# Optimization experiments

Measured on AMD Instinct MI355X. Metric: run time of the kernel, lower is better.

## Reference

```python
import jax, jax.numpy as jnp
import numpy as np
import math

INPUT_DIM = 256
HIDDEN_DIM = 128
N = 8192
GATE_TEMPERATURE = 1.0
LN_EPS = 1e-5


def setup_inputs() -> dict:
    key = jax.random.key(0)
    ks = jax.random.split(key, 10)
    s_in = 1.0 / math.sqrt(INPUT_DIM)
    s_h = 1.0 / math.sqrt(HIDDEN_DIM)
    s_cat = 1.0 / math.sqrt(INPUT_DIM + HIDDEN_DIM)
    return {
        "node_features": jax.random.normal(ks[0], (N, INPUT_DIM), jnp.float32),
        "adj_matrix": jax.random.uniform(ks[1], (N, N), jnp.float32),
        "msg_w": jax.random.uniform(ks[2], (INPUT_DIM, HIDDEN_DIM), jnp.float32, -s_in, s_in),
        "msg_b": jax.random.uniform(ks[3], (HIDDEN_DIM,), jnp.float32, -s_in, s_in),
        "upd_w": jax.random.uniform(ks[4], (INPUT_DIM + HIDDEN_DIM, HIDDEN_DIM), jnp.float32, -s_cat, s_cat),
        "upd_b": jax.random.uniform(ks[5], (HIDDEN_DIM,), jnp.float32, -s_cat, s_cat),
        "gate_q_w": jax.random.uniform(ks[6], (HIDDEN_DIM, HIDDEN_DIM), jnp.float32, -s_h, s_h),
        "gate_k_w": jax.random.uniform(ks[7], (HIDDEN_DIM, HIDDEN_DIM), jnp.float32, -s_h, s_h),
        "gate_bias": jnp.float32(-1.0),
        "ln_gamma": jnp.ones((HIDDEN_DIM,), jnp.float32),
        "ln_beta": jnp.zeros((HIDDEN_DIM,), jnp.float32),
    }


def reference(node_features, adj_matrix, msg_w, msg_b, upd_w, upd_b,
              gate_q_w, gate_k_w, gate_bias, ln_gamma, ln_beta):
    # messages: [N, hidden]
    messages = node_features @ msg_w + msg_b
    # edge gates: sigmoid(QK^T / (sqrt(d)*tau) + b), masked by adjacency
    q = messages @ gate_q_w  # [N, hidden]
    k = messages @ gate_k_w  # [N, hidden]
    scale = 1.0 / (math.sqrt(HIDDEN_DIM) * max(GATE_TEMPERATURE, 1e-6))
    scores = (q @ k.T) * scale  # [N, N]
    gates_masked = jax.nn.sigmoid(scores + gate_bias) * adj_matrix
    aggregated = gates_masked @ messages  # [N, hidden]
    combined = jnp.concatenate([node_features, aggregated], axis=1)
    updated = jax.nn.relu(combined @ upd_w + upd_b)
    # LayerNorm over last dim
    mu = jnp.mean(updated, axis=-1, keepdims=True)
    var = jnp.var(updated, axis=-1, keepdims=True)
    normed = (updated - mu) * jax.lax.rsqrt(var + LN_EPS)
    return normed * ln_gamma + ln_beta
```

## Files before the change

### kernel.cpp

```cpp
#include <hip/hip_runtime.h>
#include <hip/hip_bf16.h>
#include <stdint.h>

#define NN 8192
#define DIN 256
#define HID 128
#define SCALE 0.08838834764831845f

typedef __attribute__((ext_vector_type(8))) short short8;
typedef __attribute__((ext_vector_type(4))) float f32x4;
typedef __attribute__((ext_vector_type(8))) unsigned short u16x8;
typedef __attribute__((ext_vector_type(4))) unsigned short u16x4;

__device__ __forceinline__ unsigned short f2bf(float f) {
  unsigned int u = __builtin_bit_cast(unsigned int, f);
  u += 0x7FFFu + ((u >> 16) & 1u);
  return (unsigned short)(u >> 16);
}

__device__ __forceinline__ void async16(const void* g, void* l) {
  __builtin_amdgcn_global_load_lds(
      (const __attribute__((address_space(1))) unsigned int*)g,
      (__attribute__((address_space(3))) unsigned int*)l, 16, 0, 0);
}

__global__ __launch_bounds__(256) void kw0(
    const float* __restrict__ msg_w, const float* __restrict__ qw,
    const float* __restrict__ kw, const float* __restrict__ upd_w,
    unsigned short* __restrict__ mwT, unsigned short* __restrict__ qwT,
    unsigned short* __restrict__ kwT, unsigned short* __restrict__ w_t) {
  int idx0 = blockIdx.x * 1792 + threadIdx.x;
#pragma unroll
  for (int it = 0; it < 7; ++it) {
    int idx = idx0 + it * 256;
    if (idx < 32768) {
      int h = idx >> 8, j = idx & 255;
      mwT[idx] = f2bf(msg_w[j * HID + h]);
    } else if (idx < 49152) {
      int r = idx - 32768, h = r >> 7, j = r & 127;
      qwT[r] = f2bf(qw[j * HID + h]);
    } else if (idx < 65536) {
      int r = idx - 49152, h = r >> 7, j = r & 127;
      kwT[r] = f2bf(kw[j * HID + h]);
    } else {
      int r = idx - 65536, h = r / 384, j = r % 384;
      w_t[r] = f2bf(upd_w[j * HID + h]);
    }
  }
}

__global__ __launch_bounds__(256) void ka(
    const float* __restrict__ nf, const unsigned short* __restrict__ mwT,
    const float* __restrict__ msg_b, const unsigned short* __restrict__ qwT,
    const unsigned short* __restrict__ kwT, unsigned short* __restrict__ q_bf,
    unsigned short* __restrict__ k_bf, unsigned short* __restrict__ m_t,
    unsigned short* __restrict__ nf_bf) {
  __shared__ __align__(16) unsigned short nfl[32][264];
  __shared__ __align__(16) unsigned short ml[32][136];
  int t = threadIdx.x, l = t & 63, w = t >> 6;
  int lr = l & 15, lg = l >> 4;
  int i0 = blockIdx.x * 32;
  {
    int row = t >> 3, c0 = (t & 7) * 32;
    const float* src = nf + (size_t)(i0 + row) * DIN + c0;
    unsigned short* gdst = nf_bf + (size_t)(i0 + row) * DIN + c0;
#pragma unroll
    for (int v = 0; v < 4; ++v) {
      f32x4 a = *(const f32x4*)(src + v * 8);
      f32x4 b = *(const f32x4*)(src + v * 8 + 4);
      u16x8 o;
#pragma unroll
      for (int e = 0; e < 4; ++e) { o[e] = f2bf(a[e]); o[4 + e] = f2bf(b[e]); }
      *(u16x8*)&nfl[row][c0 + v * 8] = o;
      *(u16x8*)(gdst + v * 8) = o;
    }
  }
  __syncthreads();
  int rl = (w >> 1) * 16;
  int nb = (w & 1) * 4;
  f32x4 macc[4];
#pragma unroll
  for (int nt = 0; nt < 4; ++nt) macc[nt] = (f32x4){0.f, 0.f, 0.f, 0.f};
#pragma unroll
  for (int kk = 0; kk < 8; ++kk) {
    short8 af = *(const short8*)&nfl[rl + lr][kk * 32 + lg * 8];
#pragma unroll
    for (int nt = 0; nt < 4; ++nt) {
      short8 bf = *(const short8*)(mwT + (size_t)((nb + nt) * 16 + lr) * DIN + kk * 32 + lg * 8);
      macc[nt] = __builtin_amdgcn_mfma_f32_16x16x32_bf16(af, bf, macc[nt], 0, 0, 0);
    }
  }
#pragma unroll
  for (int nt = 0; nt < 4; ++nt) {
    int col = (nb + nt) * 16 + lr;
    float bias = msg_b[col];
#pragma unroll
    for (int reg = 0; reg < 4; ++reg)
      ml[rl + lg * 4 + reg][col] = f2bf(macc[nt][reg] + bias);
  }
  __syncthreads();
  {
    int hh = t >> 1, i8 = (t & 1) * 16;
    u16x8 o0, o1;
#pragma unroll
    for (int v = 0; v < 8; ++v) { o0[v] = ml[i8 + v][hh]; o1[v] = ml[i8 + 8 + v][hh]; }
    *(u16x8*)(m_t + (size_t)hh * NN + i0 + i8) = o0;
    *(u16x8*)(m_t + (size_t)hh * NN + i0 + i8 + 8) = o1;
  }
  f32x4 qacc[4], kacc[4];
#pragma unroll
  for (int nt = 0; nt < 4; ++nt) {
    qacc[nt] = (f32x4){0.f, 0.f, 0.f, 0.f};
    kacc[nt] = (f32x4){0.f, 0.f, 0.f, 0.f};
  }
#pragma unroll
  for (int kk = 0; kk < 4; ++kk) {
    short8 af = *(const short8*)&ml[rl + lr][kk * 32 + lg * 8];
#pragma unroll
    for (int nt = 0; nt < 4; ++nt) {
      short8 bq = *(const short8*)(qwT + (size_t)((nb + nt) * 16 + lr) * HID + kk * 32 + lg * 8);
      short8 bk = *(const short8*)(kwT + (size_t)((nb + nt) * 16 + lr) * HID + kk * 32 + lg * 8);
      qacc[nt] = __builtin_amdgcn_mfma_f32_16x16x32_bf16(af, bq, qacc[nt], 0, 0, 0);
      kacc[nt] = __builtin_amdgcn_mfma_f32_16x16x32_bf16(af, bk, kacc[nt], 0, 0, 0);
    }
  }
#pragma unroll
  for (int nt = 0; nt < 4; ++nt) {
    int col = (nb + nt) * 16 + lr;
#pragma unroll
    for (int reg = 0; reg < 4; ++reg) {
      int row = i0 + rl + lg * 4 + reg;
      q_bf[(size_t)row * HID + col] = f2bf(qacc[nt][reg]);
      k_bf[(size_t)row * HID + col] = f2bf(kacc[nt][reg]);
    }
  }
}

__global__ __launch_bounds__(256, 4) void kb(
    const unsigned short* __restrict__ q_bf, const unsigned short* __restrict__ k_bf,
    const unsigned short* __restrict__ m_t, const float* __restrict__ adj,
    const float* __restrict__ gate_bias, float* __restrict__ agg_parts) {
  __shared__ __align__(16) char klds[16384];
  __shared__ __align__(16) char mlds[16384];
  __shared__ __align__(16) char glds[8192];
  int t = threadIdx.x, l = t & 63, w = t >> 6;
  int lr = l & 15, lg = l >> 4;
  int lin = blockIdx.x + blockIdx.y * 128;
  int nlin = (lin & 7) * 128 + (lin >> 3);
  int bx = nlin & 127, by = nlin >> 7;
  int i0 = bx * 64;
  int jbase = by * 1024;
  float gb = gate_bias[0];

  int qrow = i0 + w * 16 + lr;
  short8 qf[4];
#pragma unroll
  for (int kk = 0; kk < 4; ++kk)
    qf[kk] = *(const short8*)(q_bf + (size_t)qrow * HID + kk * 32 + lg * 8);

  f32x4 acc[8];
#pragma unroll
  for (int nt = 0; nt < 8; ++nt) acc[nt] = (f32x4){0.f, 0.f, 0.f, 0.f};

  for (int jt = 0; jt < 16; ++jt) {
    int j0 = jbase + jt * 64;
    __syncthreads();
    float adjv[4][4];
#pragma unroll
    for (int jt16 = 0; jt16 < 4; ++jt16)
#pragma unroll
      for (int reg = 0; reg < 4; ++reg)
        adjv[jt16][reg] =
            adj[(size_t)(i0 + w * 16 + lg * 4 + reg) * NN + j0 + jt16 * 16 + lr];
#pragma unroll
    for (int p = 0; p < 4; ++p) {
      int row = p * 16 + (t >> 4);
      int lb = (t & 15) ^ (row & 7);
      async16(k_bf + (size_t)(j0 + row) * HID + lb * 8, klds + p * 4096 + w * 1024);
    }
#pragma unroll
    for (int p = 0; p < 4; ++p) {
      int row = p * 32 + (t >> 3);
      int lb = (t & 7) ^ (row & 7);
      async16(m_t + (size_t)row * NN + j0 + lb * 8, mlds + p * 4096 + w * 1024);
    }
    __syncthreads();

#pragma unroll
    for (int jt16 = 0; jt16 < 4; ++jt16) {
      f32x4 s_acc = (f32x4){0.f, 0.f, 0.f, 0.f};
#pragma unroll
      for (int kk = 0; kk < 4; ++kk) {
        int row = jt16 * 16 + lr;
        int blk = kk * 4 + lg;
        const short8 bf = *(const short8*)(klds + row * 256 + ((blk ^ (row & 7)) * 16));
        s_acc = __builtin_amdgcn_mfma_f32_16x16x32_bf16(qf[kk], bf, s_acc, 0, 0, 0);
      }
#pragma unroll
      for (int reg = 0; reg < 4; ++reg) {
        float x = s_acc[reg] * SCALE + gb;
        float e = __expf(-x);
        float g = adjv[jt16][reg] * __builtin_amdgcn_rcpf(1.0f + e);
        int row = lg * 4 + reg;
        int colb = (jt16 * 16 + lr) * 2;
        *(unsigned short*)(glds + w * 2048 + row * 128 + (colb ^ ((row & 7) << 4))) =
            f2bf(g);
      }
    }
#pragma unroll
    for (int kk2 = 0; kk2 < 2; ++kk2) {
      short8 af = *(const short8*)(glds + w * 2048 + lr * 128 +
                                   ((kk2 * 64 + lg * 16) ^ ((lr & 7) << 4)));
#pragma unroll
      for (int nt = 0; nt < 8; ++nt) {
        int mrow = nt * 16 + lr;
        int blk = kk2 * 4 + lg;
        const short8 bf =
            *(const short8*)(mlds + mrow * 128 + ((blk ^ (mrow & 7)) * 16));
        acc[nt] = __builtin_amdgcn_mfma_f32_16x16x32_bf16(af, bf, acc[nt], 0, 0, 0);
      }
    }
  }
  float* part = agg_parts + (size_t)by * NN * HID;
#pragma unroll
  for (int nt = 0; nt < 8; ++nt)
#pragma unroll
    for (int reg = 0; reg < 4; ++reg)
      part[(size_t)(i0 + w * 16 + lg * 4 + reg) * HID + nt * 16 + lr] = acc[nt][reg];
}

__global__ __launch_bounds__(256) void kc(
    const unsigned short* __restrict__ nf_bf, const float* __restrict__ agg_parts,
    const unsigned short* __restrict__ w_t, const float* __restrict__ upd_b,
    const float* __restrict__ gamma, const float* __restrict__ beta,
    float* __restrict__ out) {
  __shared__ __align__(16) unsigned short aggl[64][136];
  int t = threadIdx.x, l = t & 63, w = t >> 6;
  int i0 = blockIdx.x * 64;
  {
    const f32x4* p0 = (const f32x4*)(agg_parts + (size_t)i0 * HID);
    const size_t ps = (size_t)NN * HID / 4;
    for (int e = t; e < 64 * HID / 4; e += 256) {
      f32x4 s = p0[e];
#pragma unroll
      for (int c = 1; c < 8; ++c) s += p0[e + c * ps];
      int row = (e * 4) / HID, col = (e * 4) % HID;
      u16x4 o;
#pragma unroll
      for (int v = 0; v < 4; ++v) o[v] = f2bf(s[v]);
      *(u16x4*)&aggl[row][col] = o;
    }
  }
  __syncthreads();
  int lr = l & 15, lg = l >> 4;
  int arow = i0 + w * 16 + lr;
  short8 af[12];
#pragma unroll
  for (int kk = 0; kk < 8; ++kk)
    af[kk] = *(const short8*)(nf_bf + (size_t)arow * DIN + kk * 32 + lg * 8);
#pragma unroll
  for (int kk = 8; kk < 12; ++kk)
    af[kk] = *(const short8*)(&aggl[w * 16 + lr][(kk - 8) * 32 + lg * 8]);
  f32x4 acc[8];
#pragma unroll
  for (int nt = 0; nt < 8; ++nt) acc[nt] = (f32x4){0.f, 0.f, 0.f, 0.f};
#pragma unroll
  for (int kk = 0; kk < 12; ++kk)
#pragma unroll
    for (int nt = 0; nt < 8; ++nt) {
      const short8 bf =
          *(const short8*)(w_t + (size_t)(nt * 16 + lr) * 384 + kk * 32 + lg * 8);
      acc[nt] = __builtin_amdgcn_mfma_f32_16x16x32_bf16(af[kk], bf, acc[nt], 0, 0, 0);
    }
  float ub[8], ga[8], be[8];
#pragma unroll
  for (int nt = 0; nt < 8; ++nt) {
    ub[nt] = upd_b[nt * 16 + lr];
    ga[nt] = gamma[nt * 16 + lr];
    be[nt] = beta[nt * 16 + lr];
  }
  float v[8][4], sum[4], sq[4];
#pragma unroll
  for (int reg = 0; reg < 4; ++reg) { sum[reg] = 0.f; sq[reg] = 0.f; }
#pragma unroll
  for (int nt = 0; nt < 8; ++nt)
#pragma unroll
    for (int reg = 0; reg < 4; ++reg) {
      float x = acc[nt][reg] + ub[nt];
      x = fmaxf(x, 0.f);
      v[nt][reg] = x;
      sum[reg] += x;
      sq[reg] = fmaf(x, x, sq[reg]);
    }
#pragma unroll
  for (int reg = 0; reg < 4; ++reg) {
#pragma unroll
    for (int m = 1; m < 16; m <<= 1) {
      sum[reg] += __shfl_xor(sum[reg], m, 16);
      sq[reg] += __shfl_xor(sq[reg], m, 16);
    }
  }
#pragma unroll
  for (int reg = 0; reg < 4; ++reg) {
    float mu = sum[reg] * (1.0f / 128.0f);
    float var = sq[reg] * (1.0f / 128.0f) - mu * mu;
    float rstd = rsqrtf(var + 1e-5f);
    int orow = i0 + w * 16 + lg * 4 + reg;
#pragma unroll
    for (int nt = 0; nt < 8; ++nt) {
      float y = (v[nt][reg] - mu) * rstd * ga[nt] + be[nt];
      out[(size_t)orow * HID + nt * 16 + lr] = y;
    }
  }
}

extern "C" void kernel_launch(void* const* d_in, const int* in_sizes, int n_in,
                              void* d_out, int out_size, void* d_ws, size_t ws_size,
                              hipStream_t stream) {
  const float* nf    = (const float*)d_in[0];
  const float* adj   = (const float*)d_in[1];
  const float* msg_w = (const float*)d_in[2];
  const float* msg_b = (const float*)d_in[3];
  const float* upd_w = (const float*)d_in[4];
  const float* upd_b = (const float*)d_in[5];
  const float* qw    = (const float*)d_in[6];
  const float* kw    = (const float*)d_in[7];
  const float* gbias = (const float*)d_in[8];
  const float* gamma = (const float*)d_in[9];
  const float* beta  = (const float*)d_in[10];
  char* ws = (char*)d_ws;
  unsigned short* q_bf  = (unsigned short*)(ws);
  unsigned short* k_bf  = (unsigned short*)(ws + 0x200000);
  unsigned short* m_t   = (unsigned short*)(ws + 0x400000);
  unsigned short* nf_bf = (unsigned short*)(ws + 0x600000);
  unsigned short* w_t   = (unsigned short*)(ws + 0xA00000);
  unsigned short* mwT   = (unsigned short*)(ws + 0xA20000);
  unsigned short* qwT   = (unsigned short*)(ws + 0xA30000);
  unsigned short* kwT   = (unsigned short*)(ws + 0xA38000);
  float* agg            = (float*)(ws + 0xA40000);

  kw0<<<64, 256, 0, stream>>>(msg_w, qw, kw, upd_w, mwT, qwT, kwT, w_t);
  ka<<<256, 256, 0, stream>>>(nf, mwT, msg_b, qwT, kwT, q_bf, k_bf, m_t, nf_bf);
  kb<<<dim3(128, 8), 256, 0, stream>>>(q_bf, k_bf, m_t, adj, gbias, agg);
  kc<<<128, 256, 0, stream>>>(nf_bf, agg, w_t, upd_b, gamma, beta, (float*)d_out);
}
```

Baseline: 137.2 us.

## Prefetch next adjacency tile into registers and use partial vmcnt wait

Double-buffers the adjacency values in registers so the loads for the next 64-column tile are issued before the current tile's compute. The full syncthreads pair is replaced by a waitcnt that waits only for the async K/M LDS loads while the 16 adjacency loads stay in flight, followed by raw barriers. This is meant to hide the latency of the adj stream, which dominates the kernel. It depends on the compiler issuing memory ops in the expected order, which the inline vmcnt count assumes. It also adds register pressure.

```diff
diff --git a/kernel.cpp b/kernel.cpp
--- a/kernel.cpp
+++ b/kernel.cpp
@@ -158,33 +158,50 @@
   for (int kk = 0; kk < 4; ++kk)
     qf[kk] = *(const short8*)(q_bf + (size_t)qrow * HID + kk * 32 + lg * 8);
 
+  int krow = t >> 4;
+  int klb = (t & 15) ^ (krow & 7);
+  int mrow_s = t >> 3;
+  int mlb = (t & 7) ^ (mrow_s & 7);
+
+  const float* arow[4];
+#pragma unroll
+  for (int reg = 0; reg < 4; ++reg)
+    arow[reg] = adj + (size_t)(i0 + w * 16 + lg * 4 + reg) * NN + lr;
+
   f32x4 acc[8];
 #pragma unroll
   for (int nt = 0; nt < 8; ++nt) acc[nt] = (f32x4){0.f, 0.f, 0.f, 0.f};
 
+  float adjv[2][4][4];
+#pragma unroll
+  for (int jt16 = 0; jt16 < 4; ++jt16)
+#pragma unroll
+    for (int reg = 0; reg < 4; ++reg)
+      adjv[0][jt16][reg] = arow[reg][jbase + jt16 * 16];
+
+#pragma unroll 2
   for (int jt = 0; jt < 16; ++jt) {
+    const int cur = jt & 1;
     int j0 = jbase + jt * 64;
-    __syncthreads();
-    float adjv[4][4];
-#pragma unroll
-    for (int jt16 = 0; jt16 < 4; ++jt16)
-#pragma unroll
-      for (int reg = 0; reg < 4; ++reg)
-        adjv[jt16][reg] =
-            adj[(size_t)(i0 + w * 16 + lg * 4 + reg) * NN + j0 + jt16 * 16 + lr];
-#pragma unroll
-    for (int p = 0; p < 4; ++p) {
-      int row = p * 16 + (t >> 4);
-      int lb = (t & 15) ^ (row & 7);
-      async16(k_bf + (size_t)(j0 + row) * HID + lb * 8, klds + p * 4096 + w * 1024);
-    }
-#pragma unroll
-    for (int p = 0; p < 4; ++p) {
-      int row = p * 32 + (t >> 3);
-      int lb = (t & 7) ^ (row & 7);
-      async16(m_t + (size_t)row * NN + j0 + lb * 8, mlds + p * 4096 + w * 1024);
-    }
-    __syncthreads();
+#pragma unroll
+    for (int p = 0; p < 4; ++p)
+      async16(k_bf + (size_t)(j0 + p * 16 + krow) * HID + klb * 8,
+              klds + p * 4096 + w * 1024);
+#pragma unroll
+    for (int p = 0; p < 4; ++p)
+      async16(m_t + (size_t)(p * 32 + mrow_s) * NN + j0 + mlb * 8,
+              mlds + p * 4096 + w * 1024);
+    asm volatile("" ::: "memory");
+    {
+      int jn0 = jbase + (jt < 15 ? jt + 1 : jt) * 64;
+#pragma unroll
+      for (int jt16 = 0; jt16 < 4; ++jt16)
+#pragma unroll
+        for (int reg = 0; reg < 4; ++reg)
+          adjv[cur ^ 1][jt16][reg] = arow[reg][jn0 + jt16 * 16];
+    }
+    asm volatile("s_waitcnt vmcnt(16)" ::: "memory");
+    __builtin_amdgcn_s_barrier();
 
 #pragma unroll
     for (int jt16 = 0; jt16 < 4; ++jt16) {
@@ -200,7 +217,7 @@
       for (int reg = 0; reg < 4; ++reg) {
         float x = s_acc[reg] * SCALE + gb;
         float e = __expf(-x);
-        float g = adjv[jt16][reg] * __builtin_amdgcn_rcpf(1.0f + e);
+        float g = adjv[cur][jt16][reg] * __builtin_amdgcn_rcpf(1.0f + e);
         int row = lg * 4 + reg;
         int colb = (jt16 * 16 + lr) * 2;
         *(unsigned short*)(glds + w * 2048 + row * 128 + (colb ^ ((row & 7) << 4))) =
@@ -220,6 +237,7 @@
         acc[nt] = __builtin_amdgcn_mfma_f32_16x16x32_bf16(af, bf, acc[nt], 0, 0, 0);
       }
     }
+    __builtin_amdgcn_s_barrier();
   }
   float* part = agg_parts + (size_t)by * NN * HID;
 #pragma unroll
```

New measurement: 146.9 us. 7.1% more time.

## Load K and message fragments directly from global memory instead of LDS staging

Applied to the files above, without the earlier changes.

Removes the LDS staging of the K and transposed-message tiles in the gated aggregation kernel. Each wave now reads its MFMA B-fragments straight from global memory (via L1/L2), which also drops both per-iteration block barriers. This saves LDS capacity and sync overhead, but every wave re-fetches the same K and M tiles, so global/L2 traffic and latency exposure go up and there is no cross-wave reuse.

```diff
diff --git a/kernel.cpp b/kernel.cpp
--- a/kernel.cpp
+++ b/kernel.cpp
@@ -16,12 +16,6 @@
   unsigned int u = __builtin_bit_cast(unsigned int, f);
   u += 0x7FFFu + ((u >> 16) & 1u);
   return (unsigned short)(u >> 16);
-}
-
-__device__ __forceinline__ void async16(const void* g, void* l) {
-  __builtin_amdgcn_global_load_lds(
-      (const __attribute__((address_space(1))) unsigned int*)g,
-      (__attribute__((address_space(3))) unsigned int*)l, 16, 0, 0);
 }
 
 __global__ __launch_bounds__(256) void kw0(
@@ -140,8 +134,6 @@
     const unsigned short* __restrict__ q_bf, const unsigned short* __restrict__ k_bf,
     const unsigned short* __restrict__ m_t, const float* __restrict__ adj,
     const float* __restrict__ gate_bias, float* __restrict__ agg_parts) {
-  __shared__ __align__(16) char klds[16384];
-  __shared__ __align__(16) char mlds[16384];
   __shared__ __align__(16) char glds[8192];
   int t = threadIdx.x, l = t & 63, w = t >> 6;
   int lr = l & 15, lg = l >> 4;
@@ -158,42 +150,34 @@
   for (int kk = 0; kk < 4; ++kk)
     qf[kk] = *(const short8*)(q_bf + (size_t)qrow * HID + kk * 32 + lg * 8);
 
+  const float* arow[4];
+#pragma unroll
+  for (int reg = 0; reg < 4; ++reg)
+    arow[reg] = adj + (size_t)(i0 + w * 16 + lg * 4 + reg) * NN + lr;
+
+  const unsigned short* kfrag = k_bf + lr * HID + lg * 8;
+  const unsigned short* mfrag = m_t + (size_t)lr * NN + lg * 8;
+
   f32x4 acc[8];
 #pragma unroll
   for (int nt = 0; nt < 8; ++nt) acc[nt] = (f32x4){0.f, 0.f, 0.f, 0.f};
 
   for (int jt = 0; jt < 16; ++jt) {
     int j0 = jbase + jt * 64;
-    __syncthreads();
     float adjv[4][4];
 #pragma unroll
     for (int jt16 = 0; jt16 < 4; ++jt16)
 #pragma unroll
       for (int reg = 0; reg < 4; ++reg)
-        adjv[jt16][reg] =
-            adj[(size_t)(i0 + w * 16 + lg * 4 + reg) * NN + j0 + jt16 * 16 + lr];
-#pragma unroll
-    for (int p = 0; p < 4; ++p) {
-      int row = p * 16 + (t >> 4);
-      int lb = (t & 15) ^ (row & 7);
-      async16(k_bf + (size_t)(j0 + row) * HID + lb * 8, klds + p * 4096 + w * 1024);
-    }
-#pragma unroll
-    for (int p = 0; p < 4; ++p) {
-      int row = p * 32 + (t >> 3);
-      int lb = (t & 7) ^ (row & 7);
-      async16(m_t + (size_t)row * NN + j0 + lb * 8, mlds + p * 4096 + w * 1024);
-    }
-    __syncthreads();
+        adjv[jt16][reg] = arow[reg][j0 + jt16 * 16];
 
 #pragma unroll
     for (int jt16 = 0; jt16 < 4; ++jt16) {
       f32x4 s_acc = (f32x4){0.f, 0.f, 0.f, 0.f};
 #pragma unroll
       for (int kk = 0; kk < 4; ++kk) {
-        int row = jt16 * 16 + lr;
-        int blk = kk * 4 + lg;
-        const short8 bf = *(const short8*)(klds + row * 256 + ((blk ^ (row & 7)) * 16));
+        const short8 bf =
+            *(const short8*)(kfrag + (size_t)(j0 + jt16 * 16) * HID + kk * 32);
         s_acc = __builtin_amdgcn_mfma_f32_16x16x32_bf16(qf[kk], bf, s_acc, 0, 0, 0);
       }
 #pragma unroll
@@ -213,10 +197,8 @@
                                    ((kk2 * 64 + lg * 16) ^ ((lr & 7) << 4)));
 #pragma unroll
       for (int nt = 0; nt < 8; ++nt) {
-        int mrow = nt * 16 + lr;
-        int blk = kk2 * 4 + lg;
         const short8 bf =
-            *(const short8*)(mlds + mrow * 128 + ((blk ^ (mrow & 7)) * 16));
+            *(const short8*)(mfrag + (size_t)(nt * 16) * NN + j0 + kk2 * 32);
         acc[nt] = __builtin_amdgcn_mfma_f32_16x16x32_bf16(af, bf, acc[nt], 0, 0, 0);
       }
     }
```

Measured after the change: 308.5 us. +124.9%, slower.
